# Kernel optimization log

Measured on AMD Instinct MI355X. Metric: run time of the kernel, lower is better.

Reference implementation:

```python
import jax, jax.numpy as jnp
import numpy as np

N, E = 20000, 160000          # nodes, edges
D, ED, H, NH = 32, 16, 64, 4  # node_dim, edge_dim, hidden_dim, num_heads
G, MAXN = 100, 200            # graphs, nodes per graph (equal-size graphs)
HD = H // NH                  # head dim


def setup_inputs() -> dict:
    key = jax.random.key(0)
    ks = jax.random.split(key, 20)
    p = lambda k, shp: jax.random.normal(k, shp, dtype=jnp.float32) * 0.05
    return {
        "x": jax.random.normal(ks[0], (N, D), dtype=jnp.float32),
        "edge_index": jax.random.randint(ks[1], (2, E), 0, N),
        "edge_attr": jax.random.normal(ks[2], (E, ED), dtype=jnp.float32),
        "batch": jnp.arange(N, dtype=jnp.int32) // MAXN,  # 100 graphs x 200 nodes
        "en_w1": p(ks[3], (H, ED)), "en_b1": p(ks[4], (H,)),
        "en_w2": p(ks[5], (D * H, H)), "en_b2": p(ks[6], (D * H,)),
        "root_w": p(ks[7], (D, H)), "conv_b": p(ks[8], (H,)),
        "in_proj_w": p(ks[9], (3 * H, H)), "in_proj_b": p(ks[10], (3 * H,)),
        "out_proj_w": p(ks[11], (H, H)), "out_proj_b": p(ks[12], (H,)),
        "lin1_w": p(ks[13], (H, H)), "lin1_b": p(ks[14], (H,)),
        "lin2_w": p(ks[15], (1, H)), "lin2_b": p(ks[16], (1,)),
    }


def reference(x, edge_index, edge_attr, batch,
              en_w1, en_b1, en_w2, en_b2, root_w, conv_b,
              in_proj_w, in_proj_b, out_proj_w, out_proj_b,
              lin1_w, lin1_b, lin2_w, lin2_b):
    src, dst = edge_index[0], edge_index[1]
    # ---- NNConv: edge MLP -> per-edge weight [E, D, H], gather-matmul-scatter-mean ----
    h = jax.nn.relu(edge_attr @ en_w1.T + en_b1)
    w_e = (h @ en_w2.T + en_b2).reshape(E, D, H)
    msgs = jnp.einsum('ed,edh->eh', x[src], w_e)                 # [E, H]
    agg = jax.ops.segment_sum(msgs, dst, num_segments=N)         # scatter-sum by dest
    cnt = jax.ops.segment_sum(jnp.ones((E,), x.dtype), dst, num_segments=N)
    agg = agg / jnp.maximum(cnt, 1.0)[:, None]                   # mean aggregation
    xh = jax.nn.relu(agg + x @ root_w + conv_b)                  # root weight + bias
    # ---- to_dense_batch (batch is sorted) ----
    counts = jax.ops.segment_sum(jnp.ones((N,), jnp.int32), batch, num_segments=G)
    starts = jnp.concatenate([jnp.zeros((1,), jnp.int32), jnp.cumsum(counts)[:-1]])
    pos = jnp.arange(N, dtype=jnp.int32) - starts[batch]
    dense = jnp.zeros((G, MAXN, H), xh.dtype).at[batch, pos].set(xh)
    mask = jnp.zeros((G, MAXN), bool).at[batch, pos].set(True)
    # ---- MultiheadAttention (self-attn, key_padding_mask = ~mask) ----
    qkv = dense @ in_proj_w.T + in_proj_b                        # [G, MAXN, 3H]
    q, k, v = jnp.split(qkv, 3, axis=-1)
    sh = lambda t: t.reshape(G, MAXN, NH, HD).transpose(0, 2, 1, 3)  # [G, NH, MAXN, HD]
    q, k, v = sh(q), sh(k), sh(v)
    scores = jnp.einsum('gnqd,gnkd->gnqk', q, k) / jnp.sqrt(jnp.float32(HD))
    scores = jnp.where(mask[:, None, None, :], scores, jnp.float32(-1e9))
    attn = jax.nn.softmax(scores, axis=-1)
    ctx = jnp.einsum('gnqk,gnkd->gnqd', attn, v)
    ctx = ctx.transpose(0, 2, 1, 3).reshape(G, MAXN, H)
    attn_out = ctx @ out_proj_w.T + out_proj_b
    # zero out padded positions, masked mean pool
    attn_out = jnp.where(mask[:, :, None], attn_out, 0.0)
    graph_emb = attn_out.sum(axis=1) / mask.sum(axis=1, keepdims=True).astype(attn_out.dtype)
    h1 = jax.nn.relu(graph_emb @ lin1_w.T + lin1_b)
    return (h1 @ lin2_w.T + lin2_b).squeeze(1)                   # [G]
```

## Files before the change

### kernel.cpp

```cpp
#include <hip/hip_runtime.h>
#include <math.h>

#define N_N 20000
#define N_E 160000
#define KA 2112
#define NKB 66

typedef __attribute__((ext_vector_type(8))) short bfrag;
typedef __attribute__((ext_vector_type(4))) float facc;

__device__ __forceinline__ unsigned short f2bf(float f) {
  union { float f; unsigned u; } v; v.f = f;
  unsigned u = v.u;
  return (unsigned short)((u + 0x7FFF + ((u >> 16) & 1)) >> 16);
}
__device__ __forceinline__ unsigned pk2(float a, float b) {
  return (unsigned)f2bf(a) | ((unsigned)f2bf(b) << 16);
}
__device__ __forceinline__ float bflo(unsigned u) {
  union { unsigned u; float f; } v; v.u = u << 16; return v.f;
}
__device__ __forceinline__ float bfhi(unsigned u) {
  union { unsigned u; float f; } v; v.u = u & 0xffff0000u; return v.f;
}

__global__ __launch_bounds__(256) void k_mlp1(const float* __restrict__ ea,
    const float* __restrict__ w1, const float* __restrict__ b1,
    const int* __restrict__ elist, unsigned short* __restrict__ hes) {
  int t = threadIdx.x, w = t >> 6, j = t & 63;
  int p0 = blockIdx.x * 32 + w * 8;
  float wr[16];
#pragma unroll
  for (int i = 0; i < 16; ++i) wr[i] = w1[j * 16 + i];
  float bj = b1[j];
#pragma unroll
  for (int q = 0; q < 8; ++q) {
    int p = p0 + q;
    int e = elist[p];
    const float* a = ea + (size_t)e * 16;
    float s = bj;
#pragma unroll
    for (int i = 0; i < 16; ++i) s += a[i] * wr[i];
    hes[(size_t)p * 64 + j] = f2bf(fmaxf(s, 0.f));
  }
}

__global__ __launch_bounds__(256) void k_hist(const int* __restrict__ eidx,
    int* __restrict__ cnt) {
  int e = blockIdx.x * 256 + threadIdx.x;
  atomicAdd(&cnt[eidx[N_E + e]], 1);
}

__global__ __launch_bounds__(1024) void k_scan(int* __restrict__ hist,
    int* __restrict__ starts) {
  __shared__ int part[1024];
  int t = threadIdx.x;
  const int CH = 20;
  int lo = t * CH;
  int hi = lo + CH; if (hi > N_N) hi = N_N;
  int s = 0;
  for (int i = lo; i < hi; ++i) s += hist[i];
  part[t] = s;
  __syncthreads();
  for (int off = 1; off < 1024; off <<= 1) {
    int v = (t >= off) ? part[t - off] : 0;
    __syncthreads();
    part[t] += v;
    __syncthreads();
  }
  int run = (t == 0) ? 0 : part[t - 1];
  for (int i = lo; i < hi; ++i) {
    int h = hist[i];
    starts[i] = run;
    hist[i] = run;
    run += h;
  }
  if (t == 1023) starts[N_N] = part[1023];
}

__global__ __launch_bounds__(256) void k_scatter(const int* __restrict__ eidx,
    int* __restrict__ cur, int* __restrict__ elist, int* __restrict__ srcl) {
  int e = blockIdx.x * 256 + threadIdx.x;
  int dn = eidx[N_E + e];
  int pos = atomicAdd(&cur[dn], 1);
  elist[pos] = e;
  srcl[pos] = eidx[e];
}

__global__ __launch_bounds__(256) void k_pack(const float* __restrict__ w2,
    const float* __restrict__ b2f, const float* __restrict__ rootw,
    const float* __restrict__ inw,
    unsigned short* __restrict__ Bp, unsigned short* __restrict__ B2p) {
  int idx = blockIdx.x * 256 + threadIdx.x;
  if (idx < 135168) {
    int i = idx & 7, l = (idx >> 3) & 63, cbkb = idx >> 9;
    int cb = cbkb & 3, kb = cbkb >> 2;
    int r = kb * 32 + ((l >> 4) << 3) + i;
    int c = (cb << 4) + (l & 15);
    float v;
    if (r < 2048) { int d = r >> 6, k = r & 63; v = w2[((d << 6) + c) * 64 + k]; }
    else if (r < 2080) v = b2f[((r - 2048) << 6) + c];
    else v = rootw[((r - 2080) << 6) + c];
    Bp[idx] = f2bf(v);
  } else if (idx < 135168 + 12288) {
    int k2 = idx - 135168;
    int i = k2 & 7, l = (k2 >> 3) & 63, cbkb = k2 >> 9;
    int cb = cbkb % 12, kb = cbkb / 12;
    int r = kb * 32 + ((l >> 4) << 3) + i;
    int c = (cb << 4) + (l & 15);
    B2p[k2] = f2bf(inw[c * 64 + r]);
  }
}

#define FMA8(hv, base, xv) \
  acc[base + 0] += xv * bflo(hv.x); acc[base + 1] += xv * bfhi(hv.x); \
  acc[base + 2] += xv * bflo(hv.y); acc[base + 3] += xv * bfhi(hv.y); \
  acc[base + 4] += xv * bflo(hv.z); acc[base + 5] += xv * bfhi(hv.z); \
  acc[base + 6] += xv * bflo(hv.w); acc[base + 7] += xv * bfhi(hv.w);

__global__ __launch_bounds__(256, 4) void k_fused(const float* __restrict__ x,
    const unsigned short* __restrict__ hes, const int* __restrict__ starts,
    const int* __restrict__ srcl,
    const unsigned short* __restrict__ Bp, const unsigned short* __restrict__ B2p,
    const float* __restrict__ convb, const float* __restrict__ inb,
    float* __restrict__ Qb, float* __restrict__ Kb, float* __restrict__ Vb) {
  __shared__ unsigned short Ps[8 * KA];
  __shared__ unsigned short xhT[8 * 68];
  int t = threadIdx.x, w = t >> 6, l = t & 63;
  int n0 = blockIdx.x * 8;
  int d0 = l >> 3, hc = (l & 7) * 8, l31 = l & 31;
#pragma unroll 1
  for (int i4 = 0; i4 < 2; ++i4) {
    int m = w * 2 + i4;
    int n = n0 + m;
    int s0 = starts[n], s1 = starts[n + 1];
    float acc[32];
#pragma unroll
    for (int z = 0; z < 32; ++z) acc[z] = 0.f;
    float xs = 0.f;
#pragma unroll 1
    for (int c0 = s0; c0 < s1; c0 += 64) {
      int srv = 0;
      if (c0 + l < s1) srv = srcl[c0 + l];
      int cc = s1 - c0; if (cc > 64) cc = 64;
#pragma unroll 1
      for (int i = 0; i < cc; i += 4) {
        uint4 h0 = {0,0,0,0}, h1 = {0,0,0,0}, h2 = {0,0,0,0}, h3 = {0,0,0,0};
        float xv0 = 0.f, xv1 = 0.f, xv2 = 0.f, xv3 = 0.f;
        int sr0 = __shfl(srv, i);
        int sr1 = __shfl(srv, i + 1);
        int sr2 = __shfl(srv, i + 2);
        int sr3 = __shfl(srv, i + 3);
        const unsigned short* hp = hes + (size_t)(c0 + i) * 64 + hc;
        h0 = *(const uint4*)hp;
        xv0 = x[(size_t)sr0 * 32 + l31];
        if (i + 1 < cc) { h1 = *(const uint4*)(hp + 64);  xv1 = x[(size_t)sr1 * 32 + l31]; }
        if (i + 2 < cc) { h2 = *(const uint4*)(hp + 128); xv2 = x[(size_t)sr2 * 32 + l31]; }
        if (i + 3 < cc) { h3 = *(const uint4*)(hp + 192); xv3 = x[(size_t)sr3 * 32 + l31]; }
        float a0 = __shfl(xv0, d0),      a1 = __shfl(xv0, d0 + 8);
        float a2 = __shfl(xv0, d0 + 16), a3 = __shfl(xv0, d0 + 24);
        FMA8(h0, 0, a0) FMA8(h0, 8, a1) FMA8(h0, 16, a2) FMA8(h0, 24, a3)
        float b0 = __shfl(xv1, d0),      b1 = __shfl(xv1, d0 + 8);
        float b2 = __shfl(xv1, d0 + 16), b3 = __shfl(xv1, d0 + 24);
        FMA8(h1, 0, b0) FMA8(h1, 8, b1) FMA8(h1, 16, b2) FMA8(h1, 24, b3)
        float c0f = __shfl(xv2, d0),      c1f = __shfl(xv2, d0 + 8);
        float c2f = __shfl(xv2, d0 + 16), c3f = __shfl(xv2, d0 + 24);
        FMA8(h2, 0, c0f) FMA8(h2, 8, c1f) FMA8(h2, 16, c2f) FMA8(h2, 24, c3f)
        float e0 = __shfl(xv3, d0),      e1 = __shfl(xv3, d0 + 8);
        float e2 = __shfl(xv3, d0 + 16), e3 = __shfl(xv3, d0 + 24);
        FMA8(h3, 0, e0) FMA8(h3, 8, e1) FMA8(h3, 16, e2) FMA8(h3, 24, e3)
        xs += xv0 + xv1 + xv2 + xv3;
      }
    }
    int s = m;
#pragma unroll
    for (int q = 0; q < 4; ++q) {
      int sc = (l + 64 * q) ^ s;
      uint4 o;
      o.x = pk2(acc[q * 8 + 0], acc[q * 8 + 1]);
      o.y = pk2(acc[q * 8 + 2], acc[q * 8 + 3]);
      o.z = pk2(acc[q * 8 + 4], acc[q * 8 + 5]);
      o.w = pk2(acc[q * 8 + 6], acc[q * 8 + 7]);
      *(uint4*)(Ps + m * KA + sc * 8) = o;
    }
    if (l < 32) {
      int cnt = s1 - s0; if (cnt < 1) cnt = 1;
      int c1 = (256 + (l >> 3)) ^ s, c2 = (260 + (l >> 3)) ^ s;
      Ps[m * KA + c1 * 8 + (l & 7)] = f2bf(xs);
      Ps[m * KA + c2 * 8 + (l & 7)] = f2bf(x[(size_t)n * 32 + l] * (float)cnt);
    }
  }
  __syncthreads();
  int col = l & 15, sub = l >> 4;
  int arow = col & 7;
  const bfrag* Bb = (const bfrag*)Bp + w * 64 + l;
  facc ac = {0.f, 0.f, 0.f, 0.f};
#pragma unroll 4
  for (int kb = 0; kb < NKB; ++kb) {
    int sc = ((kb << 2) + sub) ^ arow;
    bfrag af = *(const bfrag*)(Ps + arow * KA + sc * 8);
    ac = __builtin_amdgcn_mfma_f32_16x16x32_bf16(af, Bb[kb * 256], ac, 0, 0, 0);
  }
  float cv = convb[w * 16 + col];
#pragma unroll
  for (int j = 0; j < 4; ++j) {
    int m = sub * 4 + j;
    if (m < 8) {
      int n = n0 + m;
      int cnt = starts[n + 1] - starts[n]; if (cnt < 1) cnt = 1;
      float inv = 1.f / (float)cnt;
      xhT[m * 68 + w * 16 + col] = f2bf(fmaxf(ac[j] * inv + cv, 0.f));
    }
  }
  __syncthreads();
  bfrag af0 = *(const bfrag*)&xhT[(col & 7) * 68 + sub * 8];
  bfrag af1 = *(const bfrag*)&xhT[(col & 7) * 68 + 32 + sub * 8];
  const bfrag* B2b = (const bfrag*)B2p + l;
#pragma unroll
  for (int c3 = 0; c3 < 3; ++c3) {
    int cb = w * 3 + c3;
    facc qa = {0.f, 0.f, 0.f, 0.f};
    qa = __builtin_amdgcn_mfma_f32_16x16x32_bf16(af0, B2b[cb * 64], qa, 0, 0, 0);
    qa = __builtin_amdgcn_mfma_f32_16x16x32_bf16(af1, B2b[(12 + cb) * 64], qa, 0, 0, 0);
#pragma unroll
    for (int j = 0; j < 4; ++j) {
      int m = sub * 4 + j;
      if (m < 8) {
        int n = n0 + m;
        int g = n / 200, p = n - g * 200;
        int c = cb * 16 + col;
        float v = qa[j] + inb[c];
        int part = c >> 6, rem = c & 63, hh = rem >> 4, dd = rem & 15;
        float* dst = (part == 0) ? Qb : (part == 1 ? Kb : Vb);
        dst[(((size_t)g * 4 + hh) * 200 + p) * 16 + dd] = v;
      }
    }
  }
}

__global__ __launch_bounds__(256) void k_attn(const float* __restrict__ Qb,
    const float* __restrict__ Kb, const float* __restrict__ Vb,
    float* __restrict__ ctx) {
  __shared__ unsigned short Ks[224 * 24];
  __shared__ unsigned short Vt[16 * 232];
  __shared__ unsigned short Pl[4][16 * 40];
  int t = threadIdx.x;
  int gh = blockIdx.x >> 1, half = blockIdx.x & 1;
  size_t base = (size_t)gh * 3200;
  for (int idx = t; idx < 224 * 16; idx += 256) {
    int row = idx >> 4, d = idx & 15;
    float kv = (row < 200) ? Kb[base + idx] : 0.f;
    float vv = (row < 200) ? Vb[base + idx] : 0.f;
    Ks[row * 24 + d] = f2bf(kv);
    Vt[d * 232 + row] = f2bf(vv);
  }
  __syncthreads();
  int w = t >> 6, l = t & 63;
  int sub = l >> 4, col = l & 15;
  int qlo = half * 7, qhi = half ? 13 : 7;
  for (int qt = qlo + w; qt < qhi; qt += 4) {
    bfrag qf = {0, 0, 0, 0, 0, 0, 0, 0};
    int q = qt * 16 + col;
    if (sub < 2 && q < 200) {
      const float* qp = Qb + base + q * 16 + sub * 8;
      float4 qa = *(const float4*)qp;
      float4 qb = *(const float4*)(qp + 4);
      qf[0] = (short)f2bf(qa.x); qf[1] = (short)f2bf(qa.y);
      qf[2] = (short)f2bf(qa.z); qf[3] = (short)f2bf(qa.w);
      qf[4] = (short)f2bf(qb.x); qf[5] = (short)f2bf(qb.y);
      qf[6] = (short)f2bf(qb.z); qf[7] = (short)f2bf(qb.w);
    }
    facc o = {0.f, 0.f, 0.f, 0.f};
    float srow0 = 0.f, srow1 = 0.f, srow2 = 0.f, srow3 = 0.f;
    for (int kt2 = 0; kt2 < 7; ++kt2) {
      int kt0 = kt2 * 2, kt1 = kt0 + 1;
      bfrag kf0 = {0, 0, 0, 0, 0, 0, 0, 0};
      bfrag kf1 = {0, 0, 0, 0, 0, 0, 0, 0};
      if (sub < 2) {
        kf0 = *(const bfrag*)&Ks[(kt0 * 16 + col) * 24 + sub * 8];
        kf1 = *(const bfrag*)&Ks[(kt1 * 16 + col) * 24 + sub * 8];
      }
      facc z = {0.f, 0.f, 0.f, 0.f};
      facc s0 = __builtin_amdgcn_mfma_f32_16x16x32_bf16(qf, kf0, z, 0, 0, 0);
      facc s1 = __builtin_amdgcn_mfma_f32_16x16x32_bf16(qf, kf1, z, 0, 0, 0);
      bool ok0 = (kt0 * 16 + col) < 200;
      bool ok1 = (kt1 * 16 + col) < 200;
#pragma unroll
      for (int j = 0; j < 4; ++j) {
        float e0 = ok0 ? __expf(s0[j] * 0.25f) : 0.f;
        float e1 = ok1 ? __expf(s1[j] * 0.25f) : 0.f;
        if (j == 0) { srow0 += e0 + e1; } else if (j == 1) { srow1 += e0 + e1; }
        else if (j == 2) { srow2 += e0 + e1; } else { srow3 += e0 + e1; }
        int qr = (sub << 2) + j;
        Pl[w][qr * 40 + col] = f2bf(e0);
        Pl[w][qr * 40 + 16 + col] = f2bf(e1);
      }
      bfrag pf = *(const bfrag*)&Pl[w][col * 40 + sub * 8];
      bfrag vf = *(const bfrag*)&Vt[col * 232 + kt2 * 32 + sub * 8];
      o = __builtin_amdgcn_mfma_f32_16x16x32_bf16(pf, vf, o, 0, 0, 0);
    }
#pragma unroll
    for (int off = 1; off < 16; off <<= 1) {
      srow0 += __shfl_xor(srow0, off);
      srow1 += __shfl_xor(srow1, off);
      srow2 += __shfl_xor(srow2, off);
      srow3 += __shfl_xor(srow3, off);
    }
#pragma unroll
    for (int j = 0; j < 4; ++j) {
      int qq = qt * 16 + (sub << 2) + j;
      float sr = (j == 0) ? srow0 : (j == 1) ? srow1 : (j == 2) ? srow2 : srow3;
      if (qq < 200) ctx[base + qq * 16 + col] = o[j] / sr;
    }
  }
}

__global__ __launch_bounds__(256) void k_head(const float* __restrict__ ctx,
    const float* __restrict__ ow, const float* __restrict__ ob,
    const float* __restrict__ w1, const float* __restrict__ b1,
    const float* __restrict__ w2, const float* __restrict__ b2,
    float* __restrict__ out) {
  __shared__ float pool[4][64];
  __shared__ float ms[64], es[64];
  int g = blockIdx.x, t = threadIdx.x;
  int q = t >> 6, c = t & 63;
  int hh = c >> 4, dd = c & 15;
  const float* cb = ctx + (((size_t)g * 4 + hh) * 200) * 16 + dd;
  float s = 0.f;
  for (int p = q; p < 200; p += 4) s += cb[p * 16];
  pool[q][c] = s;
  __syncthreads();
  if (t < 64) {
    float sm = pool[0][t] + pool[1][t] + pool[2][t] + pool[3][t];
    ms[t] = sm * (1.f / 200.f);
  }
  __syncthreads();
  if (t < 64) {
    float e = ob[t];
    for (int j = 0; j < 64; ++j) e += ow[t * 64 + j] * ms[j];
    es[t] = e;
  }
  __syncthreads();
  if (t < 64) {
    float h1 = b1[t];
    for (int j = 0; j < 64; ++j) h1 += w1[t * 64 + j] * es[j];
    h1 = fmaxf(h1, 0.f);
    float pr = h1 * w2[t];
    for (int off = 32; off >= 1; off >>= 1) pr += __shfl_xor(pr, off);
    if (t == 0) out[g] = pr + b2[0];
  }
}

extern "C" void kernel_launch(void* const* d_in, const int* in_sizes, int n_in,
                              void* d_out, int out_size, void* d_ws, size_t ws_size,
                              hipStream_t stream) {
  (void)in_sizes; (void)n_in;
  const float* x      = (const float*)d_in[0];
  const int*   eidx   = (const int*)d_in[1];
  const float* ea     = (const float*)d_in[2];
  const float* en_w1  = (const float*)d_in[4];
  const float* en_b1  = (const float*)d_in[5];
  const float* en_w2  = (const float*)d_in[6];
  const float* en_b2  = (const float*)d_in[7];
  const float* root_w = (const float*)d_in[8];
  const float* conv_b = (const float*)d_in[9];
  const float* in_w   = (const float*)d_in[10];
  const float* in_b   = (const float*)d_in[11];
  const float* out_w  = (const float*)d_in[12];
  const float* out_b  = (const float*)d_in[13];
  const float* l1w    = (const float*)d_in[14];
  const float* l1b    = (const float*)d_in[15];
  const float* l2w    = (const float*)d_in[16];
  const float* l2b    = (const float*)d_in[17];
  float* out = (float*)d_out;

  char* w = (char*)d_ws;
  unsigned short* hes = (unsigned short*)w;
  float* Qb  = (float*)(w + 20480000);
  float* Kb  = (float*)(w + 25600000);
  float* Vb  = (float*)(w + 30720000);
  float* ctx = (float*)(w + 35840000);
  char* r3 = w + 40960000;
  unsigned short* Bp  = (unsigned short*)r3;
  unsigned short* B2p = (unsigned short*)(r3 + 270336);
  int* starts = (int*)(r3 + 270336 + 24576);
  int* elist  = starts + (N_N + 4);
  int* srcl   = elist + N_E;
  int* cursor = srcl + N_E;
  size_t need = 40960000 + 270336 + 24576
              + (size_t)(N_N + 4) * 4 + 2 * (size_t)N_E * 4 + (size_t)N_N * 4;
  if (ws_size < need || out_size < 100) return;

  hipMemsetAsync(cursor, 0, N_N * 4, stream);
  k_pack<<<580, 256, 0, stream>>>(en_w2, en_b2, root_w, in_w, Bp, B2p);
  k_hist<<<N_E / 256, 256, 0, stream>>>(eidx, cursor);
  k_scan<<<1, 1024, 0, stream>>>(cursor, starts);
  k_scatter<<<N_E / 256, 256, 0, stream>>>(eidx, cursor, elist, srcl);
  k_mlp1<<<5000, 256, 0, stream>>>(ea, en_w1, en_b1, elist, hes);
  k_fused<<<2500, 256, 0, stream>>>(x, hes, starts, srcl, Bp, B2p,
                                    conv_b, in_b, Qb, Kb, Vb);
  k_attn<<<800, 256, 0, stream>>>(Qb, Kb, Vb, ctx);
  k_head<<<100, 256, 0, stream>>>(ctx, out_w, out_b, l1w, l1b, l2w, l2b, out);
}
```

Before: 180.7 us.

## Fuse mean-pool into attention, fold memset into pack, widen fused gather blocks

Three separate changes. The attention kernel now reduces its context outputs per graph and atomically adds them into a small pool buffer, so the full ctx tensor is no longer written and then reread by the head kernel, which shrinks to 64 threads. The cursor memset is folded into the pack kernel, along with zeroing of the pool buffer. The fused NNConv kernel now runs 512 threads with one node per wave instead of two nodes per wave in sequence, which adds parallelism on the gather but leaves half the waves idle during the MFMA phases.

```diff
diff --git a/kernel.cpp b/kernel.cpp
--- a/kernel.cpp
+++ b/kernel.cpp
@@ -90,8 +90,10 @@
 __global__ __launch_bounds__(256) void k_pack(const float* __restrict__ w2,
     const float* __restrict__ b2f, const float* __restrict__ rootw,
     const float* __restrict__ inw,
-    unsigned short* __restrict__ Bp, unsigned short* __restrict__ B2p) {
+    unsigned short* __restrict__ Bp, unsigned short* __restrict__ B2p,
+    int* __restrict__ cursor, float* __restrict__ pool) {
   int idx = blockIdx.x * 256 + threadIdx.x;
+  const int GT = 580 * 256;
   if (idx < 135168) {
     int i = idx & 7, l = (idx >> 3) & 63, cbkb = idx >> 9;
     int cb = cbkb & 3, kb = cbkb >> 2;
@@ -110,6 +112,8 @@
     int c = (cb << 4) + (l & 15);
     B2p[k2] = f2bf(inw[c * 64 + r]);
   }
+  for (int i = idx; i < N_N; i += GT) cursor[i] = 0;
+  for (int i = idx; i < 6400; i += GT) pool[i] = 0.f;
 }
 
 #define FMA8(hv, base, xv) \
@@ -118,7 +122,7 @@
   acc[base + 4] += xv * bflo(hv.z); acc[base + 5] += xv * bfhi(hv.z); \
   acc[base + 6] += xv * bflo(hv.w); acc[base + 7] += xv * bfhi(hv.w);
 
-__global__ __launch_bounds__(256, 4) void k_fused(const float* __restrict__ x,
+__global__ __launch_bounds__(512, 8) void k_fused(const float* __restrict__ x,
     const unsigned short* __restrict__ hes, const int* __restrict__ starts,
     const int* __restrict__ srcl,
     const unsigned short* __restrict__ Bp, const unsigned short* __restrict__ B2p,
@@ -129,9 +133,8 @@
   int t = threadIdx.x, w = t >> 6, l = t & 63;
   int n0 = blockIdx.x * 8;
   int d0 = l >> 3, hc = (l & 7) * 8, l31 = l & 31;
-#pragma unroll 1
-  for (int i4 = 0; i4 < 2; ++i4) {
-    int m = w * 2 + i4;
+  {
+    int m = w;
     int n = n0 + m;
     int s0 = starts[n], s1 = starts[n + 1];
     float acc[32];
@@ -175,13 +178,13 @@
     int s = m;
 #pragma unroll
     for (int q = 0; q < 4; ++q) {
-      int sc = (l + 64 * q) ^ s;
+      int scr = (l + 64 * q) ^ s;
       uint4 o;
       o.x = pk2(acc[q * 8 + 0], acc[q * 8 + 1]);
       o.y = pk2(acc[q * 8 + 2], acc[q * 8 + 3]);
       o.z = pk2(acc[q * 8 + 4], acc[q * 8 + 5]);
       o.w = pk2(acc[q * 8 + 6], acc[q * 8 + 7]);
-      *(uint4*)(Ps + m * KA + sc * 8) = o;
+      *(uint4*)(Ps + m * KA + scr * 8) = o;
     }
     if (l < 32) {
       int cnt = s1 - s0; if (cnt < 1) cnt = 1;
@@ -193,46 +196,50 @@
   __syncthreads();
   int col = l & 15, sub = l >> 4;
   int arow = col & 7;
-  const bfrag* Bb = (const bfrag*)Bp + w * 64 + l;
-  facc ac = {0.f, 0.f, 0.f, 0.f};
+  if (w < 4) {
+    const bfrag* Bb = (const bfrag*)Bp + w * 64 + l;
+    facc ac = {0.f, 0.f, 0.f, 0.f};
 #pragma unroll 4
-  for (int kb = 0; kb < NKB; ++kb) {
-    int sc = ((kb << 2) + sub) ^ arow;
-    bfrag af = *(const bfrag*)(Ps + arow * KA + sc * 8);
-    ac = __builtin_amdgcn_mfma_f32_16x16x32_bf16(af, Bb[kb * 256], ac, 0, 0, 0);
-  }
-  float cv = convb[w * 16 + col];
-#pragma unroll
-  for (int j = 0; j < 4; ++j) {
-    int m = sub * 4 + j;
-    if (m < 8) {
-      int n = n0 + m;
-      int cnt = starts[n + 1] - starts[n]; if (cnt < 1) cnt = 1;
-      float inv = 1.f / (float)cnt;
-      xhT[m * 68 + w * 16 + col] = f2bf(fmaxf(ac[j] * inv + cv, 0.f));
-    }
-  }
-  __syncthreads();
-  bfrag af0 = *(const bfrag*)&xhT[(col & 7) * 68 + sub * 8];
-  bfrag af1 = *(const bfrag*)&xhT[(col & 7) * 68 + 32 + sub * 8];
-  const bfrag* B2b = (const bfrag*)B2p + l;
-#pragma unroll
-  for (int c3 = 0; c3 < 3; ++c3) {
-    int cb = w * 3 + c3;
-    facc qa = {0.f, 0.f, 0.f, 0.f};
-    qa = __builtin_amdgcn_mfma_f32_16x16x32_bf16(af0, B2b[cb * 64], qa, 0, 0, 0);
-    qa = __builtin_amdgcn_mfma_f32_16x16x32_bf16(af1, B2b[(12 + cb) * 64], qa, 0, 0, 0);
+    for (int kb = 0; kb < NKB; ++kb) {
+      int scr = ((kb << 2) + sub) ^ arow;
+      bfrag af = *(const bfrag*)(Ps + arow * KA + scr * 8);
+      ac = __builtin_amdgcn_mfma_f32_16x16x32_bf16(af, Bb[kb * 256], ac, 0, 0, 0);
+    }
+    float cv = convb[w * 16 + col];
 #pragma unroll
     for (int j = 0; j < 4; ++j) {
       int m = sub * 4 + j;
       if (m < 8) {
         int n = n0 + m;
-        int g = n / 200, p = n - g * 200;
-        int c = cb * 16 + col;
-        float v = qa[j] + inb[c];
-        int part = c >> 6, rem = c & 63, hh = rem >> 4, dd = rem & 15;
-        float* dst = (part == 0) ? Qb : (part == 1 ? Kb : Vb);
-        dst[(((size_t)g * 4 + hh) * 200 + p) * 16 + dd] = v;
+        int cnt = starts[n + 1] - starts[n]; if (cnt < 1) cnt = 1;
+        float inv = 1.f / (float)cnt;
+        xhT[m * 68 + w * 16 + col] = f2bf(fmaxf(ac[j] * inv + cv, 0.f));
+      }
+    }
+  }
+  __syncthreads();
+  if (w < 4) {
+    bfrag af0 = *(const bfrag*)&xhT[(col & 7) * 68 + sub * 8];
+    bfrag af1 = *(const bfrag*)&xhT[(col & 7) * 68 + 32 + sub * 8];
+    const bfrag* B2b = (const bfrag*)B2p + l;
+#pragma unroll
+    for (int c3 = 0; c3 < 3; ++c3) {
+      int cb = w * 3 + c3;
+      facc qa = {0.f, 0.f, 0.f, 0.f};
+      qa = __builtin_amdgcn_mfma_f32_16x16x32_bf16(af0, B2b[cb * 64], qa, 0, 0, 0);
+      qa = __builtin_amdgcn_mfma_f32_16x16x32_bf16(af1, B2b[(12 + cb) * 64], qa, 0, 0, 0);
+#pragma unroll
+      for (int j = 0; j < 4; ++j) {
+        int m = sub * 4 + j;
+        if (m < 8) {
+          int n = n0 + m;
+          int g = n / 200, p = n - g * 200;
+          int c = cb * 16 + col;
+          float v = qa[j] + inb[c];
+          int part = c >> 6, rem = c & 63, hh = rem >> 4, dd = rem & 15;
+          float* dst = (part == 0) ? Qb : (part == 1 ? Kb : Vb);
+          dst[(((size_t)g * 4 + hh) * 200 + p) * 16 + dd] = v;
+        }
       }
     }
   }
@@ -240,10 +247,11 @@
 
 __global__ __launch_bounds__(256) void k_attn(const float* __restrict__ Qb,
     const float* __restrict__ Kb, const float* __restrict__ Vb,
-    float* __restrict__ ctx) {
+    float* __restrict__ pool) {
   __shared__ unsigned short Ks[224 * 24];
   __shared__ unsigned short Vt[16 * 232];
   __shared__ unsigned short Pl[4][16 * 40];
+  __shared__ float pw[4][16];
   int t = threadIdx.x;
   int gh = blockIdx.x >> 1, half = blockIdx.x & 1;
   size_t base = (size_t)gh * 3200;
@@ -258,6 +266,7 @@
   int w = t >> 6, l = t & 63;
   int sub = l >> 4, col = l & 15;
   int qlo = half * 7, qhi = half ? 13 : 7;
+  float pacc = 0.f;
   for (int qt = qlo + w; qt < qhi; qt += 4) {
     bfrag qf = {0, 0, 0, 0, 0, 0, 0, 0};
     int q = qt * 16 + col;
@@ -310,45 +319,38 @@
     for (int j = 0; j < 4; ++j) {
       int qq = qt * 16 + (sub << 2) + j;
       float sr = (j == 0) ? srow0 : (j == 1) ? srow1 : (j == 2) ? srow2 : srow3;
-      if (qq < 200) ctx[base + qq * 16 + col] = o[j] / sr;
-    }
-  }
-}
-
-__global__ __launch_bounds__(256) void k_head(const float* __restrict__ ctx,
+      if (qq < 200) pacc += o[j] / sr;
+    }
+  }
+  pacc += __shfl_xor(pacc, 16);
+  pacc += __shfl_xor(pacc, 32);
+  if (l < 16) pw[w][l] = pacc;
+  __syncthreads();
+  if (t < 16) {
+    float v = pw[0][t] + pw[1][t] + pw[2][t] + pw[3][t];
+    atomicAdd(&pool[gh * 16 + t], v);
+  }
+}
+
+__global__ __launch_bounds__(64) void k_head(const float* __restrict__ pool,
     const float* __restrict__ ow, const float* __restrict__ ob,
     const float* __restrict__ w1, const float* __restrict__ b1,
     const float* __restrict__ w2, const float* __restrict__ b2,
     float* __restrict__ out) {
-  __shared__ float pool[4][64];
   __shared__ float ms[64], es[64];
   int g = blockIdx.x, t = threadIdx.x;
-  int q = t >> 6, c = t & 63;
-  int hh = c >> 4, dd = c & 15;
-  const float* cb = ctx + (((size_t)g * 4 + hh) * 200) * 16 + dd;
-  float s = 0.f;
-  for (int p = q; p < 200; p += 4) s += cb[p * 16];
-  pool[q][c] = s;
-  __syncthreads();
-  if (t < 64) {
-    float sm = pool[0][t] + pool[1][t] + pool[2][t] + pool[3][t];
-    ms[t] = sm * (1.f / 200.f);
-  }
-  __syncthreads();
-  if (t < 64) {
-    float e = ob[t];
-    for (int j = 0; j < 64; ++j) e += ow[t * 64 + j] * ms[j];
-    es[t] = e;
-  }
-  __syncthreads();
-  if (t < 64) {
-    float h1 = b1[t];
-    for (int j = 0; j < 64; ++j) h1 += w1[t * 64 + j] * es[j];
-    h1 = fmaxf(h1, 0.f);
-    float pr = h1 * w2[t];
-    for (int off = 32; off >= 1; off >>= 1) pr += __shfl_xor(pr, off);
-    if (t == 0) out[g] = pr + b2[0];
-  }
+  ms[t] = pool[g * 64 + t] * (1.f / 200.f);
+  __syncthreads();
+  float e = ob[t];
+  for (int j = 0; j < 64; ++j) e += ow[t * 64 + j] * ms[j];
+  es[t] = e;
+  __syncthreads();
+  float h1 = b1[t];
+  for (int j = 0; j < 64; ++j) h1 += w1[t * 64 + j] * es[j];
+  h1 = fmaxf(h1, 0.f);
+  float pr = h1 * w2[t];
+  for (int off = 32; off >= 1; off >>= 1) pr += __shfl_xor(pr, off);
+  if (t == 0) out[g] = pr + b2[0];
 }
 
 extern "C" void kernel_launch(void* const* d_in, const int* in_sizes, int n_in,
@@ -379,26 +381,25 @@
   float* Qb  = (float*)(w + 20480000);
   float* Kb  = (float*)(w + 25600000);
   float* Vb  = (float*)(w + 30720000);
-  float* ctx = (float*)(w + 35840000);
-  char* r3 = w + 40960000;
+  float* pool = (float*)(w + 35840000);
+  char* r3 = w + 35870000;
   unsigned short* Bp  = (unsigned short*)r3;
   unsigned short* B2p = (unsigned short*)(r3 + 270336);
   int* starts = (int*)(r3 + 270336 + 24576);
   int* elist  = starts + (N_N + 4);
   int* srcl   = elist + N_E;
   int* cursor = srcl + N_E;
-  size_t need = 40960000 + 270336 + 24576
+  size_t need = 35870000 + 270336 + 24576
               + (size_t)(N_N + 4) * 4 + 2 * (size_t)N_E * 4 + (size_t)N_N * 4;
   if (ws_size < need || out_size < 100) return;
 
-  hipMemsetAsync(cursor, 0, N_N * 4, stream);
-  k_pack<<<580, 256, 0, stream>>>(en_w2, en_b2, root_w, in_w, Bp, B2p);
+  k_pack<<<580, 256, 0, stream>>>(en_w2, en_b2, root_w, in_w, Bp, B2p, cursor, pool);
   k_hist<<<N_E / 256, 256, 0, stream>>>(eidx, cursor);
   k_scan<<<1, 1024, 0, stream>>>(cursor, starts);
   k_scatter<<<N_E / 256, 256, 0, stream>>>(eidx, cursor, elist, srcl);
   k_mlp1<<<5000, 256, 0, stream>>>(ea, en_w1, en_b1, elist, hes);
-  k_fused<<<2500, 256, 0, stream>>>(x, hes, starts, srcl, Bp, B2p,
+  k_fused<<<2500, 512, 0, stream>>>(x, hes, starts, srcl, Bp, B2p,
                                     conv_b, in_b, Qb, Kb, Vb);
-  k_attn<<<800, 256, 0, stream>>>(Qb, Kb, Vb, ctx);
-  k_head<<<100, 256, 0, stream>>>(ctx, out_w, out_b, l1w, l1b, l2w, l2b, out);
-}
+  k_attn<<<800, 256, 0, stream>>>(Qb, Kb, Vb, pool);
+  k_head<<<100, 64, 0, stream>>>(pool, out_w, out_b, l1w, l1b, l2w, l2b, out);
+}
```

After: 297.7 us. 64.8% more time.
